# Optimization experiments

Measured on AMD Instinct MI355X. Metric: run time of the kernel, lower is better.

The kernel has to match this reference:

```python
import jax, jax.numpy as jnp
import numpy as np

N_NODES = 100000
N_FEAT = 128
HIDDEN = 64
OUT = 16
N_EDGES = 3200000
N_POS = 500000
N_NEG = 500000


def setup_inputs() -> dict:
    key = jax.random.key(0)
    ks = jax.random.split(key, 8)
    x = jax.random.normal(ks[0], (N_NODES, N_FEAT), dtype=jnp.float32)
    edge_index = jax.random.randint(ks[1], (2, N_EDGES), 0, N_NODES, dtype=jnp.int64)
    pos_edge_index = jax.random.randint(ks[2], (2, N_POS), 0, N_NODES, dtype=jnp.int64)
    neg_edge_index = jax.random.randint(ks[3], (2, N_NEG), 0, N_NODES, dtype=jnp.int64)
    W1 = jax.random.normal(ks[4], (N_FEAT, HIDDEN), dtype=jnp.float32) * (1.0 / np.sqrt(N_FEAT))
    b1 = jnp.zeros((HIDDEN,), dtype=jnp.float32)
    W2 = jax.random.normal(ks[5], (HIDDEN, OUT), dtype=jnp.float32) * (1.0 / np.sqrt(HIDDEN))
    b2 = jnp.zeros((OUT,), dtype=jnp.float32)
    return {"x": x, "edge_index": edge_index, "pos_edge_index": pos_edge_index,
            "neg_edge_index": neg_edge_index, "W1": W1, "b1": b1, "W2": W2, "b2": b2}


def gcn_conv(x, W, b, src, dst):
    """PyG GCNConv with add_self_loops=True: D^-1/2 (A+I) D^-1/2 X W + b."""
    n = x.shape[0]
    h = x @ W  # [N, out]
    # degree including self-loop (+1)
    deg = jax.ops.segment_sum(jnp.ones(dst.shape, dtype=h.dtype), dst, num_segments=n) + 1.0
    dis = jax.lax.rsqrt(deg)  # deg >= 1, never inf
    coef = dis[src] * dis[dst]  # [E]
    agg = jax.ops.segment_sum(h[src] * coef[:, None], dst, num_segments=n)
    # self-loop message: norm = dis[i]*dis[i]
    agg = agg + h * (dis * dis)[:, None]
    return agg + b


def reference(x, edge_index, pos_edge_index, neg_edge_index, W1, b1, W2, b2):
    src, dst = edge_index[0], edge_index[1]
    z = jax.nn.relu(gcn_conv(x, W1, b1, src, dst))
    z = gcn_conv(z, W2, b2, src, dst)  # [N, 16]
    ei = jnp.concatenate([pos_edge_index, neg_edge_index], axis=-1)  # [2, P+Q]
    logits = jnp.sum(z[ei[0]] * z[ei[1]], axis=-1)  # [P+Q]
    return logits
```

## Files before the change

### kernel.cpp

```cpp
#include <hip/hip_runtime.h>

#define F 128
#define H 64
#define O 16

#define BSHIFT 7
#define BSZ 128
#define NSUB 16
#define SUBCAP 384
#define ACHUNK 8192
#define XS 136

typedef _Float16 half8_t __attribute__((ext_vector_type(8)));
typedef _Float16 half4_t __attribute__((ext_vector_type(4)));
typedef float f32x4 __attribute__((ext_vector_type(4)));

#define MIX2(alo, ahi, dw)                                                              \
    do {                                                                                \
        asm("v_fma_mix_f32 %0, %1, 1.0, %0 op_sel_hi:[1,0,0]"                           \
            : "+v"(alo) : "v"(dw));                                                     \
        asm("v_fma_mix_f32 %0, %1, 1.0, %0 op_sel:[1,0,0] op_sel_hi:[1,0,0]"            \
            : "+v"(ahi) : "v"(dw));                                                     \
    } while (0)

#define MIXROW(r)                                                                       \
    do {                                                                                \
        MIX2(acc[0], acc[1], (r).x);                                                    \
        MIX2(acc[2], acc[3], (r).y);                                                    \
        MIX2(acc[4], acc[5], (r).z);                                                    \
        MIX2(acc[6], acc[7], (r).w);                                                    \
    } while (0)

__global__ void k_prep(const float* __restrict__ W1, _Float16* __restrict__ wt_hi,
                       _Float16* __restrict__ wt_lo, int* __restrict__ bcur, int NC) {
    int i = blockIdx.x * blockDim.x + threadIdx.x;
    if (i < NC) bcur[i] = i * SUBCAP;
    if (i < H * F) {
        int c = i >> 7, k = i & 127;
        float w = W1[k * H + c];
        _Float16 hi = (_Float16)w;
        wt_hi[i] = hi;
        wt_lo[i] = (_Float16)(w - (float)hi);
    }
}

__global__ __launch_bounds__(512) void k_bucketA(const int* __restrict__ src,
                                                 const int* __restrict__ dstv,
                                                 int* __restrict__ bcur,
                                                 int* __restrict__ bdata, int E) {
    __shared__ int hist[1024];
    for (int t = threadIdx.x; t < 1024; t += 512) hist[t] = 0;
    __syncthreads();
    int base = blockIdx.x * ACHUNK;
    int end = min(base + ACHUNK, E);
    int tid = threadIdx.x;
    int4 s4r[4], d4r[4];
    bool ok[4];
#pragma unroll
    for (int k = 0; k < 4; k++) {
        int i = base + tid * 4 + k * 2048;
        ok[k] = (i + 3 < end);
        if (ok[k]) {
            d4r[k] = *(const int4*)(dstv + i);
            s4r[k] = *(const int4*)(src + i);
            atomicAdd(&hist[d4r[k].x >> BSHIFT], 1);
            atomicAdd(&hist[d4r[k].y >> BSHIFT], 1);
            atomicAdd(&hist[d4r[k].z >> BSHIFT], 1);
            atomicAdd(&hist[d4r[k].w >> BSHIFT], 1);
        }
    }
    for (int i = base + ((end - base) & ~3) + tid; i < end; i += 512)
        atomicAdd(&hist[dstv[i] >> BSHIFT], 1);
    __syncthreads();
    int sub = blockIdx.x & (NSUB - 1);
    for (int b = tid; b < 1024; b += 512) {
        int c = hist[b];
        if (c > 0) hist[b] = atomicAdd(&bcur[b * NSUB + sub], c);
    }
    __syncthreads();
#pragma unroll
    for (int k = 0; k < 4; k++) {
        if (ok[k]) {
            int4 s4 = s4r[k];
            int4 d4 = d4r[k];
            int p0 = atomicAdd(&hist[d4.x >> BSHIFT], 1);
            bdata[p0] = (s4.x << BSHIFT) | (d4.x & (BSZ - 1));
            int p1 = atomicAdd(&hist[d4.y >> BSHIFT], 1);
            bdata[p1] = (s4.y << BSHIFT) | (d4.y & (BSZ - 1));
            int p2 = atomicAdd(&hist[d4.z >> BSHIFT], 1);
            bdata[p2] = (s4.z << BSHIFT) | (d4.z & (BSZ - 1));
            int p3 = atomicAdd(&hist[d4.w >> BSHIFT], 1);
            bdata[p3] = (s4.w << BSHIFT) | (d4.w & (BSZ - 1));
        }
    }
    for (int i = base + ((end - base) & ~3) + tid; i < end; i += 512) {
        int d = dstv[i];
        int pos = atomicAdd(&hist[d >> BSHIFT], 1);
        bdata[pos] = (src[i] << BSHIFT) | (d & (BSZ - 1));
    }
}

__global__ void k_bscan(const int* __restrict__ bcur, int* __restrict__ bstart, int NBK) {
    __shared__ int s[1024];
    int tid = threadIdx.x;
    int tot = 0;
    if (tid < NBK) {
        for (int ss = 0; ss < NSUB; ss++)
            tot += bcur[tid * NSUB + ss] - (tid * NSUB + ss) * SUBCAP;
    }
    s[tid] = tot;
    __syncthreads();
    for (int off = 1; off < 1024; off <<= 1) {
        int v = (tid >= off) ? s[tid - off] : 0;
        __syncthreads();
        s[tid] += v;
        __syncthreads();
    }
    bstart[tid] = s[tid] - tot;
}

__global__ __launch_bounds__(256) void k_bplace(const int* __restrict__ bdata,
                                                const int* __restrict__ bcur,
                                                const int* __restrict__ bstart,
                                                int* __restrict__ row_ptr,
                                                float* __restrict__ dis,
                                                int* __restrict__ col, int N) {
    __shared__ int h[BSZ];
    __shared__ int pref[BSZ];
    __shared__ int cur[BSZ];
    int b = blockIdx.x;
    int node0 = b << BSHIFT;
    int nloc = min(BSZ, N - node0);
    int tid = threadIdx.x;
    if (tid < BSZ) h[tid] = 0;
    __syncthreads();
    for (int s = 0; s < NSUB; s++) {
        int start = (b * NSUB + s) * SUBCAP;
        int end = bcur[b * NSUB + s];
        for (int p = start + tid; p < end; p += 256)
            atomicAdd(&h[bdata[p] & (BSZ - 1)], 1);
    }
    __syncthreads();
    int myDeg = 0;
    if (tid < BSZ) {
        myDeg = h[tid];
        pref[tid] = myDeg;
    }
    __syncthreads();
    for (int off = 1; off < BSZ; off <<= 1) {
        int v = (tid < BSZ && tid >= off) ? pref[tid - off] : 0;
        __syncthreads();
        if (tid < BSZ) pref[tid] += v;
        __syncthreads();
    }
    int base = bstart[b];
    if (tid < nloc) {
        int excl = base + pref[tid] - myDeg;
        cur[tid] = excl;
        row_ptr[node0 + tid] = excl;
        dis[node0 + tid] = rsqrtf((float)myDeg + 1.0f);
    }
    if (tid == 0) row_ptr[node0 + nloc] = base + pref[BSZ - 1];
    __syncthreads();
    for (int s = 0; s < NSUB; s++) {
        int start = (b * NSUB + s) * SUBCAP;
        int end = bcur[b * NSUB + s];
        for (int p = start + tid; p < end; p += 256) {
            int v = bdata[p];
            int pos = atomicAdd(&cur[v & (BSZ - 1)], 1);
            col[pos] = v >> BSHIFT;
        }
    }
}

__global__ __launch_bounds__(256) void k_gemm1(const float* __restrict__ x,
                                               const _Float16* __restrict__ wt_hi,
                                               const _Float16* __restrict__ wt_lo,
                                               const float* __restrict__ dis,
                                               _Float16* __restrict__ h1p, int N) {
    __shared__ _Float16 xh[64 * XS], xl[64 * XS], wh[64 * XS], wl[64 * XS];
    int tid = threadIdx.x;
    int row0 = blockIdx.x * 64;
#pragma unroll
    for (int i = 0; i < 8; i++) {
        int idx = i * 256 + tid;
        int r = idx >> 5;
        int c = (idx & 31) * 4;
        int rr = row0 + r; if (rr >= N) rr = N - 1;
        float4 v = *(const float4*)(x + (size_t)rr * F + c);
        half4_t h = {(_Float16)v.x, (_Float16)v.y, (_Float16)v.z, (_Float16)v.w};
        half4_t l = {(_Float16)(v.x - (float)h[0]), (_Float16)(v.y - (float)h[1]),
                     (_Float16)(v.z - (float)h[2]), (_Float16)(v.w - (float)h[3])};
        *(half4_t*)(xh + r * XS + c) = h;
        *(half4_t*)(xl + r * XS + c) = l;
    }
#pragma unroll
    for (int i = 0; i < 4; i++) {
        int idx = i * 256 + tid;
        int c = idx >> 4;
        int k8 = (idx & 15) * 8;
        *(half8_t*)(wh + c * XS + k8) = *(const half8_t*)(wt_hi + c * 128 + k8);
        *(half8_t*)(wl + c * XS + k8) = *(const half8_t*)(wt_lo + c * 128 + k8);
    }
    __syncthreads();
    int wv = tid >> 6, lane = tid & 63;
    int m = lane & 15, qd = lane >> 4;
    const _Float16* xhp = xh + (wv * 16 + m) * XS;
    const _Float16* xlp = xl + (wv * 16 + m) * XS;
    f32x4 acc[4] = {f32x4{0,0,0,0}, f32x4{0,0,0,0}, f32x4{0,0,0,0}, f32x4{0,0,0,0}};
#pragma unroll
    for (int kc = 0; kc < 4; kc++) {
        int ko = kc * 32 + qd * 8;
        half8_t ah = *(const half8_t*)(xhp + ko);
        half8_t al = *(const half8_t*)(xlp + ko);
#pragma unroll
        for (int nt = 0; nt < 4; nt++) {
            half8_t bh = *(const half8_t*)(wh + (nt * 16 + m) * XS + ko);
            half8_t bl = *(const half8_t*)(wl + (nt * 16 + m) * XS + ko);
            acc[nt] = __builtin_amdgcn_mfma_f32_16x16x32_f16(ah, bh, acc[nt], 0, 0, 0);
            acc[nt] = __builtin_amdgcn_mfma_f32_16x16x32_f16(ah, bl, acc[nt], 0, 0, 0);
            acc[nt] = __builtin_amdgcn_mfma_f32_16x16x32_f16(al, bh, acc[nt], 0, 0, 0);
        }
    }
#pragma unroll
    for (int reg = 0; reg < 4; reg++) {
        int row = row0 + wv * 16 + qd * 4 + reg;
        if (row < N) {
            float d = dis[row];
#pragma unroll
            for (int nt = 0; nt < 4; nt++) {
                h1p[(size_t)row * H + nt * 16 + m] = (_Float16)(acc[nt][reg] * d);
            }
        }
    }
}

__global__ __launch_bounds__(256) void k_gather1(const _Float16* __restrict__ h1p,
                                                 const float* __restrict__ dis,
                                                 const int* __restrict__ row_ptr,
                                                 const int* __restrict__ col,
                                                 const float* __restrict__ b1,
                                                 const float* __restrict__ W2,
                                                 _Float16* __restrict__ h2p, int N) {
    __shared__ float w2t[16 * 65];
    int tid = threadIdx.x;
    {
        int idx = tid * 4;
        float4 v = *(const float4*)(W2 + idx);
        const float* vp = (const float*)&v;
#pragma unroll
        for (int i = 0; i < 4; i++) {
            int e = idx + i;
            w2t[(e & 15) * 65 + (e >> 4)] = vp[i];
        }
    }
    __syncthreads();
    int lane = tid & 63;
    int g = lane >> 3;
    int t = lane & 7;
    unsigned t16 = (unsigned)t * 16;
    const char* hb = (const char*)h1p;
    float bb[8];
#pragma unroll
    for (int j = 0; j < 8; j++) bb[j] = b1[t * 8 + j];
    float w1v[8], w2v[8];
#pragma unroll
    for (int j = 0; j < 8; j++) {
        w1v[j] = w2t[g * 65 + t * 8 + j];
        w2v[j] = w2t[(g + 8) * 65 + t * 8 + j];
    }

    for (int node = blockIdx.x * 4 + (tid >> 6); node < N; node += gridDim.x * 4) {
        float acc[8];
#pragma unroll
        for (int j = 0; j < 8; j++) acc[j] = 0.f;
        int e = row_ptr[node + 1];
        int p = row_ptr[node] + g;
        for (; p + 24 < e; p += 32) {
            int s0 = col[p], s1 = col[p + 8], s2 = col[p + 16], s3 = col[p + 24];
            int4 r0 = *(const int4*)(hb + (((unsigned)s0 << 7) + t16));
            int4 r1 = *(const int4*)(hb + (((unsigned)s1 << 7) + t16));
            int4 r2 = *(const int4*)(hb + (((unsigned)s2 << 7) + t16));
            int4 r3 = *(const int4*)(hb + (((unsigned)s3 << 7) + t16));
            MIXROW(r0); MIXROW(r1); MIXROW(r2); MIXROW(r3);
        }
        for (; p + 8 < e; p += 16) {
            int s0 = col[p], s1 = col[p + 8];
            int4 r0 = *(const int4*)(hb + (((unsigned)s0 << 7) + t16));
            int4 r1 = *(const int4*)(hb + (((unsigned)s1 << 7) + t16));
            MIXROW(r0); MIXROW(r1);
        }
        if (p < e) {
            int s0 = col[p];
            int4 r0 = *(const int4*)(hb + (((unsigned)s0 << 7) + t16));
            MIXROW(r0);
        }
        if (g == 0) {
            int4 rs = *(const int4*)(hb + (((unsigned)node << 7) + t16));
            MIXROW(rs);
        }
#pragma unroll
        for (int off = 8; off < 64; off <<= 1) {
#pragma unroll
            for (int j = 0; j < 8; j++) acc[j] += __shfl_xor(acc[j], off);
        }
        float dn = dis[node];
        float o[8];
#pragma unroll
        for (int j = 0; j < 8; j++)
            o[j] = fmaxf(fmaf(acc[j], dn, bb[j]), 0.f);
        float p1 = 0.f, p2 = 0.f;
#pragma unroll
        for (int j = 0; j < 8; j++) {
            p1 = fmaf(o[j], w1v[j], p1);
            p2 = fmaf(o[j], w2v[j], p2);
        }
#pragma unroll
        for (int off = 1; off < 8; off <<= 1) {
            p1 += __shfl_xor(p1, off);
            p2 += __shfl_xor(p2, off);
        }
        if (t == 0) {
            h2p[(size_t)node * O + g]     = (_Float16)(p1 * dn);
            h2p[(size_t)node * O + g + 8] = (_Float16)(p2 * dn);
        }
    }
}

__global__ __launch_bounds__(256) void k_gather2(const _Float16* __restrict__ h2p,
                                                 const float* __restrict__ dis,
                                                 const int* __restrict__ row_ptr,
                                                 const int* __restrict__ col,
                                                 const float* __restrict__ b2,
                                                 float* __restrict__ z2, int N) {
    int tid = threadIdx.x;
    int lane = tid & 63;
    int g = lane >> 1;
    int t = lane & 1;
    unsigned t16 = (unsigned)t * 16;
    const char* hb = (const char*)h2p;
    float bb[8];
#pragma unroll
    for (int j = 0; j < 8; j++) bb[j] = b2[t * 8 + j];

    for (int node = blockIdx.x * 4 + (tid >> 6); node < N; node += gridDim.x * 4) {
        float acc[8];
#pragma unroll
        for (int j = 0; j < 8; j++) acc[j] = 0.f;
        int e = row_ptr[node + 1];
        for (int p = row_ptr[node] + g; p < e; p += 32) {
            int s = col[p];
            int4 r = *(const int4*)(hb + (((unsigned)s << 5) + t16));
            MIXROW(r);
        }
        if (g == 0) {
            int4 rs = *(const int4*)(hb + (((unsigned)node << 5) + t16));
            MIXROW(rs);
        }
#pragma unroll
        for (int off = 2; off < 64; off <<= 1) {
#pragma unroll
            for (int j = 0; j < 8; j++) acc[j] += __shfl_xor(acc[j], off);
        }
        if (g == 0) {
            float dn = dis[node];
            float o[8];
#pragma unroll
            for (int j = 0; j < 8; j++)
                o[j] = fmaf(acc[j], dn, bb[j]);
            float4* zp = (float4*)(z2 + (size_t)node * O + t * 8);
            zp[0] = float4{o[0], o[1], o[2], o[3]};
            zp[1] = float4{o[4], o[5], o[6], o[7]};
        }
    }
}

__global__ __launch_bounds__(256) void k_logits(const float* __restrict__ z2,
                                                const int* __restrict__ pos,
                                                const int* __restrict__ neg,
                                                float* __restrict__ out, int P, int Q) {
    int tid = blockIdx.x * 256 + threadIdx.x;
    int i = tid >> 2;
    if (i >= P + Q) return;
    int k = tid & 3;
    unsigned k16 = (unsigned)k * 16;
    const char* zb = (const char*)z2;
    int a, b;
    if (i < P) { a = pos[i]; b = pos[P + i]; }
    else       { int t = i - P; a = neg[t]; b = neg[Q + t]; }
    float4 va = *(const float4*)(zb + (((unsigned)a << 6) + k16));
    float4 vb = *(const float4*)(zb + (((unsigned)b << 6) + k16));
    float r = va.x * vb.x + va.y * vb.y + va.z * vb.z + va.w * vb.w;
    r += __shfl_xor(r, 1);
    r += __shfl_xor(r, 2);
    if (k == 0) out[i] = r;
}

extern "C" void kernel_launch(void* const* d_in, const int* in_sizes, int n_in,
                              void* d_out, int out_size, void* d_ws, size_t ws_size,
                              hipStream_t stream) {
    const float* x   = (const float*)d_in[0];
    const int*   ei  = (const int*)d_in[1];
    const int*   pos = (const int*)d_in[2];
    const int*   neg = (const int*)d_in[3];
    const float* W1  = (const float*)d_in[4];
    const float* b1  = (const float*)d_in[5];
    const float* W2  = (const float*)d_in[6];
    const float* b2  = (const float*)d_in[7];
    float* out = (float*)d_out;

    int N = in_sizes[0] / F;
    int E = in_sizes[1] / 2;
    int P = in_sizes[2] / 2;
    int Q = in_sizes[3] / 2;
    const int* src  = ei;
    const int* dstv = ei + E;

    int Npad = ((N + 255) / 256) * 256;
    int Epad = (E + 63) & ~63;
    int NBK = (N + BSZ - 1) / BSZ;
    int NC  = NBK * NSUB;

    char* w = (char*)d_ws;
    float*    dis     = (float*)w;    w += (size_t)Npad * 4;
    int*      row_ptr = (int*)w;      w += (size_t)(Npad + 256) * 4;
    int*      bcur    = (int*)w;      w += 16384 * 4;
    int*      bstart  = (int*)w;      w += 1024 * 4;
    int*      col     = (int*)w;      w += (size_t)Epad * 4;
    _Float16* h1p     = (_Float16*)w;
    int*      bdata   = (int*)w;
    size_t h1b = (size_t)N * H * 2, bdb = (size_t)NC * SUBCAP * 4;
    w += (h1b > bdb ? h1b : bdb);
    _Float16* h2p     = (_Float16*)w; w += (size_t)N * O * 2;
    float*    z2      = (float*)w;    w += (size_t)N * O * 4;
    _Float16* wt_hi   = (_Float16*)w; w += (size_t)H * F * 2;
    _Float16* wt_lo   = (_Float16*)w;

    int prepN = (NC > H * F) ? NC : H * F;

    k_prep<<<(prepN + 255) / 256, 256, 0, stream>>>(W1, wt_hi, wt_lo, bcur, NC);
    k_bucketA<<<(E + ACHUNK - 1) / ACHUNK, 512, 0, stream>>>(src, dstv, bcur, bdata, E);
    k_bscan<<<1, 1024, 0, stream>>>(bcur, bstart, NBK);
    k_bplace<<<NBK, 256, 0, stream>>>(bdata, bcur, bstart, row_ptr, dis, col, N);

    k_gemm1<<<(N + 63) / 64, 256, 0, stream>>>(x, wt_hi, wt_lo, dis, h1p, N);
    k_gather1<<<2048, 256, 0, stream>>>(h1p, dis, row_ptr, col, b1, W2, h2p, N);
    k_gather2<<<(N + 3) / 4, 256, 0, stream>>>(h2p, dis, row_ptr, col, b2, z2, N);
    k_logits<<<((P + Q) * 4 + 255) / 256, 256, 0, stream>>>(z2, pos, neg, out, P, Q);
}
```

Measured before the change: 310.1 us.

## Process two nodes per wave in layer-1 gather and use wave-shuffle block scan

The layer-1 gather kernel now splits each 64-lane wave into two half-waves, each aggregating a different node with 4 edge groups instead of 8. The halves exchange their ReLU outputs so each lane can compute the 64->16 projection for both nodes. This is meant to cut wasted lanes on low-degree nodes and halve the serial reduction depth. Separately, the bucket scan replaces a shared-memory Hillis-Steele scan that needed many barriers with wave-level shuffle-up scans plus a small per-wave sum table. The gather change adds shuffle and FMA work per node and has a boundary edge case where the partner node lies past N.

```diff
diff --git a/kernel.cpp b/kernel.cpp
--- a/kernel.cpp
+++ b/kernel.cpp
@@ -101,22 +101,25 @@
 }
 
 __global__ void k_bscan(const int* __restrict__ bcur, int* __restrict__ bstart, int NBK) {
-    __shared__ int s[1024];
-    int tid = threadIdx.x;
+    __shared__ int wsum[16];
+    int tid = threadIdx.x;
+    int lane = tid & 63, wv = tid >> 6;
     int tot = 0;
     if (tid < NBK) {
         for (int ss = 0; ss < NSUB; ss++)
             tot += bcur[tid * NSUB + ss] - (tid * NSUB + ss) * SUBCAP;
     }
-    s[tid] = tot;
-    __syncthreads();
-    for (int off = 1; off < 1024; off <<= 1) {
-        int v = (tid >= off) ? s[tid - off] : 0;
-        __syncthreads();
-        s[tid] += v;
-        __syncthreads();
-    }
-    bstart[tid] = s[tid] - tot;
+    int val = tot;
+#pragma unroll
+    for (int off = 1; off < 64; off <<= 1) {
+        int u = __shfl_up(val, off);
+        if (lane >= off) val += u;
+    }
+    if (lane == 63) wsum[wv] = val;
+    __syncthreads();
+    int add = 0;
+    for (int j = 0; j < wv; j++) add += wsum[j];
+    bstart[tid] = val + add - tot;
 }
 
 __global__ __launch_bounds__(256) void k_bplace(const int* __restrict__ bdata,
@@ -256,10 +259,13 @@
     }
     __syncthreads();
     int lane = tid & 63;
+    int h = lane >> 5;
+    int g2 = (lane >> 3) & 3;
     int g = lane >> 3;
     int t = lane & 7;
     unsigned t16 = (unsigned)t * 16;
     const char* hb = (const char*)h1p;
+    int hsign = 1 - 2 * h;
     float bb[8];
 #pragma unroll
     for (int j = 0; j < 8; j++) bb[j] = b1[t * 8 + j];
@@ -270,22 +276,22 @@
         w2v[j] = w2t[(g + 8) * 65 + t * 8 + j];
     }
 
-    for (int node = blockIdx.x * 4 + (tid >> 6); node < N; node += gridDim.x * 4) {
+    for (int node = blockIdx.x * 8 + (tid >> 6) * 2 + h; node < N; node += gridDim.x * 8) {
         float acc[8];
 #pragma unroll
         for (int j = 0; j < 8; j++) acc[j] = 0.f;
         int e = row_ptr[node + 1];
-        int p = row_ptr[node] + g;
-        for (; p + 24 < e; p += 32) {
-            int s0 = col[p], s1 = col[p + 8], s2 = col[p + 16], s3 = col[p + 24];
+        int p = row_ptr[node] + g2;
+        for (; p + 12 < e; p += 16) {
+            int s0 = col[p], s1 = col[p + 4], s2 = col[p + 8], s3 = col[p + 12];
             int4 r0 = *(const int4*)(hb + (((unsigned)s0 << 7) + t16));
             int4 r1 = *(const int4*)(hb + (((unsigned)s1 << 7) + t16));
             int4 r2 = *(const int4*)(hb + (((unsigned)s2 << 7) + t16));
             int4 r3 = *(const int4*)(hb + (((unsigned)s3 << 7) + t16));
             MIXROW(r0); MIXROW(r1); MIXROW(r2); MIXROW(r3);
         }
-        for (; p + 8 < e; p += 16) {
-            int s0 = col[p], s1 = col[p + 8];
+        for (; p + 4 < e; p += 8) {
+            int s0 = col[p], s1 = col[p + 4];
             int4 r0 = *(const int4*)(hb + (((unsigned)s0 << 7) + t16));
             int4 r1 = *(const int4*)(hb + (((unsigned)s1 << 7) + t16));
             MIXROW(r0); MIXROW(r1);
@@ -295,12 +301,12 @@
             int4 r0 = *(const int4*)(hb + (((unsigned)s0 << 7) + t16));
             MIXROW(r0);
         }
-        if (g == 0) {
+        if (g2 == 0) {
             int4 rs = *(const int4*)(hb + (((unsigned)node << 7) + t16));
             MIXROW(rs);
         }
 #pragma unroll
-        for (int off = 8; off < 64; off <<= 1) {
+        for (int off = 8; off < 32; off <<= 1) {
 #pragma unroll
             for (int j = 0; j < 8; j++) acc[j] += __shfl_xor(acc[j], off);
         }
@@ -309,20 +315,33 @@
 #pragma unroll
         for (int j = 0; j < 8; j++)
             o[j] = fmaxf(fmaf(acc[j], dn, bb[j]), 0.f);
-        float p1 = 0.f, p2 = 0.f;
+        float oo[8];
+#pragma unroll
+        for (int j = 0; j < 8; j++) oo[j] = __shfl_xor(o[j], 32);
+        float dno = __shfl_xor(dn, 32);
+        float p1o = 0.f, p2o = 0.f, p1x = 0.f, p2x = 0.f;
 #pragma unroll
         for (int j = 0; j < 8; j++) {
-            p1 = fmaf(o[j], w1v[j], p1);
-            p2 = fmaf(o[j], w2v[j], p2);
+            p1o = fmaf(o[j], w1v[j], p1o);
+            p2o = fmaf(o[j], w2v[j], p2o);
+            p1x = fmaf(oo[j], w1v[j], p1x);
+            p2x = fmaf(oo[j], w2v[j], p2x);
         }
 #pragma unroll
         for (int off = 1; off < 8; off <<= 1) {
-            p1 += __shfl_xor(p1, off);
-            p2 += __shfl_xor(p2, off);
+            p1o += __shfl_xor(p1o, off);
+            p2o += __shfl_xor(p2o, off);
+            p1x += __shfl_xor(p1x, off);
+            p2x += __shfl_xor(p2x, off);
         }
         if (t == 0) {
-            h2p[(size_t)node * O + g]     = (_Float16)(p1 * dn);
-            h2p[(size_t)node * O + g + 8] = (_Float16)(p2 * dn);
+            h2p[(size_t)node * O + g]     = (_Float16)(p1o * dn);
+            h2p[(size_t)node * O + g + 8] = (_Float16)(p2o * dn);
+            int nodeo = node + hsign;
+            if (nodeo < N) {
+                h2p[(size_t)nodeo * O + g]     = (_Float16)(p1x * dno);
+                h2p[(size_t)nodeo * O + g + 8] = (_Float16)(p2x * dno);
+            }
         }
     }
 }
```

After: 306.5 us, median of 2. Within noise of the previous version (-1.2%).
